# Kernel optimization log

Hardware: AMD Instinct MI355X
Metric: run time of the kernel (lower is better)

The kernel has to match this reference:

```python
import jax, jax.numpy as jnp
import numpy as np

H, HD = 4, 32      # num_heads, head_dim
EPS = 1e-6         # flax LayerNorm default epsilon


def _ln(x, s, b):
    mu = jnp.mean(x, -1, keepdims=True)
    var = jnp.var(x, -1, keepdims=True)
    return (x - mu) * jax.lax.rsqrt(var + EPS) * s + b


def _pos_enc(T, D, dtype):
    # standard sinusoidal time-series positional encoding
    pos = jnp.arange(T, dtype=jnp.float32)[:, None]
    div = jnp.exp(-jnp.log(10000.0) * jnp.arange(0, D, 2, dtype=jnp.float32) / D)
    ang = pos * div
    pe = jnp.zeros((T, D), jnp.float32).at[:, 0::2].set(jnp.sin(ang)).at[:, 1::2].set(jnp.cos(ang))
    return pe.astype(dtype)


def _transformer(x, Wi, bi, Wqkv, bqkv, Wo, bo, l1s, l1b, l2s, l2b, W1, b1, W2, b2):
    # x: [B, T, in_dim] -> [B, T, D]; pre-LN transformer block with pos-enc
    B, T, _ = x.shape
    x = x @ Wi + bi
    D = x.shape[-1]
    x = x + _pos_enc(T, D, x.dtype)
    h = _ln(x, l1s, l1b)
    qkv = (h @ Wqkv + bqkv).reshape(B, T, 3, H, HD)
    q, k, v = qkv[:, :, 0], qkv[:, :, 1], qkv[:, :, 2]
    s = jnp.einsum('bthd,bshd->bhts', q, k) * (1.0 / np.sqrt(HD))
    o = jnp.einsum('bhts,bshd->bthd', jax.nn.softmax(s, -1), v).reshape(B, T, H * HD)
    x = x + (o @ Wo + bo)
    h = _ln(x, l2s, l2b)
    return x + jax.nn.gelu(h @ W1 + b1) @ W2 + b2


def _grand(h, Win, bin_, Wqk, bqk, Wout, bout, t_grid):
    # GRAND-style attention diffusion across node axis: dz/dt = (A(z) - I) z,
    # explicit Euler on the given time grid. h: [B, T, N, D]
    B, T, N, D = h.shape
    z = h @ Win + bin_
    dts = t_grid[1:] - t_grid[:-1]
    scale = 1.0 / np.sqrt(HD)
    for i in range(int(dts.shape[0])):
        qk = (z @ Wqk + bqk).reshape(B, T, N, 2, H, HD)
        q, k = qk[:, :, :, 0], qk[:, :, :, 1]
        s = jnp.einsum('btnhd,btmhd->bthnm', q, k) * scale
        A = jax.nn.softmax(s, -1).mean(axis=2)  # head-averaged [B, T, N, N]
        z = z + dts[i] * (jnp.einsum('btnm,btmd->btnd', A, z) - z)
    return z @ Wout + bout


def _forward(x, tt_Wi, tt_bi, tt_Wqkv, tt_bqkv, tt_Wo, tt_bo, tt_ln1s, tt_ln1b,
             tt_ln2s, tt_ln2b, tt_W1, tt_b1, tt_W2, tt_b2,
             g_Win, g_bin, g_Wqk, g_bqk, g_Wout, g_bout,
             ln_s, ln_b, mW1, mb1, mW2, mb2):
    # per-channel temporal transformer: vmap over node axis 2, params axis 0
    tmodel = jax.vmap(_transformer, in_axes=(2,) + (0,) * 14, out_axes=2)
    h = tmodel(x, tt_Wi, tt_bi, tt_Wqkv, tt_bqkv, tt_Wo, tt_bo,
               tt_ln1s, tt_ln1b, tt_ln2s, tt_ln2b, tt_W1, tt_b1, tt_W2, tt_b2)
    t_grid = jnp.linspace(0.0, 0.5, 4)
    h = _grand(h, g_Win, g_bin, g_Wqk, g_bqk, g_Wout, g_bout, t_grid)
    h2 = _ln(h, ln_s, ln_b)
    return jax.nn.gelu(h2 @ mW1 + mb1) @ mW2 + mb2


def setup_inputs() -> dict:
    key = jax.random.key(0)
    ks = iter(jax.random.split(key, 32))
    B, T, N, IN, D = 8, 128, 64, 32, 128
    w = lambda shape: jax.random.normal(next(ks), shape, jnp.float32) * 0.02
    z = lambda shape: jnp.zeros(shape, jnp.float32)
    o = lambda shape: jnp.ones(shape, jnp.float32)
    return dict(
        x=jax.random.normal(next(ks), (B, T, N, IN), jnp.float32),
        tt_Wi=w((N, IN, D)), tt_bi=z((N, D)),
        tt_Wqkv=w((N, D, 3 * H * HD)), tt_bqkv=z((N, 3 * H * HD)),
        tt_Wo=w((N, H * HD, D)), tt_bo=z((N, D)),
        tt_ln1s=o((N, D)), tt_ln1b=z((N, D)),
        tt_ln2s=o((N, D)), tt_ln2b=z((N, D)),
        tt_W1=w((N, D, D)), tt_b1=z((N, D)),
        tt_W2=w((N, D, D)), tt_b2=z((N, D)),
        g_Win=w((D, D)), g_bin=z((D,)),
        g_Wqk=w((D, 2 * H * HD)), g_bqk=z((2 * H * HD,)),
        g_Wout=w((D, D)), g_bout=z((D,)),
        ln_s=o((D,)), ln_b=z((D,)),
        mW1=w((D, D)), mb1=z((D,)),
        mW2=w((D, D)), mb2=z((D,)),
    )


def reference(x, tt_Wi, tt_bi, tt_Wqkv, tt_bqkv, tt_Wo, tt_bo, tt_ln1s, tt_ln1b,
              tt_ln2s, tt_ln2b, tt_W1, tt_b1, tt_W2, tt_b2,
              g_Win, g_bin, g_Wqk, g_bqk, g_Wout, g_bout,
              ln_s, ln_b, mW1, mb1, mW2, mb2):
    return _forward(x, tt_Wi, tt_bi, tt_Wqkv, tt_bqkv, tt_Wo, tt_bo, tt_ln1s, tt_ln1b,
                    tt_ln2s, tt_ln2b, tt_W1, tt_b1, tt_W2, tt_b2,
                    g_Win, g_bin, g_Wqk, g_bqk, g_Wout, g_bout,
                    ln_s, ln_b, mW1, mb1, mW2, mb2)
```

## Files before the change

kernel.cpp:

```cpp
#include <hip/hip_runtime.h>
#include <hip/hip_bf16.h>

using bf16 = __hip_bfloat16;
typedef __attribute__((ext_vector_type(8))) short short8;
typedef __attribute__((ext_vector_type(4))) float f32x4;


__device__ __forceinline__ bool isbf(const void* p) {
    return *(const unsigned*)p == 0x3F803F80u;
}
template <bool BF>
__device__ __forceinline__ float ldT(const void* p, size_t i) {
    if constexpr (BF) return __bfloat162float(((const bf16*)p)[i]);
    else              return ((const float*)p)[i];
}
template <bool BF>
__device__ __forceinline__ void stT(void* p, size_t i, float v) {
    if constexpr (BF) ((bf16*)p)[i] = __float2bfloat16(v);
    else              ((float*)p)[i] = v;
}
template <bool BF>
__device__ __forceinline__ unsigned ldbits(const void* p, size_t i) {
    if constexpr (BF) return ((const unsigned short*)p)[i];
    else {
// ... 50 lines not shown
            sq  += e[kk][j] * e[kk][j];
        }
    }
    sum += __shfl_xor(sum, 16); sum += __shfl_xor(sum, 32);
    sq  += __shfl_xor(sq, 16);  sq  += __shfl_xor(sq, 32);
    float mu = sum * (1.0f / 128.0f);
    float var = sq * (1.0f / 128.0f) - mu * mu;
    float rs = rsqrtf(var + 1e-6f);
#pragma unroll
    for (int kk = 0; kk < 4; ++kk) {
        unsigned dw[4];
#pragma unroll
        for (int p = 0; p < 4; ++p) {
            int col = 32 * kk + 8 * lg + 2 * p;
            float2 sv = ld2T<BF>(lnsP, pb + col);
            float2 bv = ld2T<BF>(lnbP, pb + col);
            dw[p] = pack2((e[kk][2 * p]     - mu) * rs * sv.x + bv.x,
                          (e[kk][2 * p + 1] - mu) * rs * sv.y + bv.y);
        }
        af[kk] = u4_to_s8(make_uint4(dw[0], dw[1], dw[2], dw[3]));
    }
}

template <bool BF>
__device__ __forceinline__ void repack_body(const void* __restrict__ W,
                                            uint4* __restrict__ Wf, int Nout) {
    int kk = blockIdx.x, nt = blockIdx.y, node = blockIdx.z;
    int KK = gridDim.x, NT = gridDim.y;
    int l = threadIdx.x, lg = l >> 4, li = l & 15;
    int col = nt * 16 + li;
    int k0 = kk * 32 + lg * 8;
    size_t base = (size_t)node * (KK * 32) * Nout;
    unsigned w[4];
#pragma unroll
    for (int p = 0; p < 4; ++p) {
        unsigned lo = ldbits<BF>(W, base + (size_t)(k0 + 2 * p) * Nout + col);
        unsigned hi = ldbits<BF>(W, base + (size_t)(k0 + 2 * p + 1) * Nout + col);
        w[p] = lo | (hi << 16);
    }
    Wf[(((size_t)node * NT + nt) * KK + kk) * 64 + l] =
        make_uint4(w[0], w[1], w[2], w[3]);
}
__global__ __launch_bounds__(64) void k_repack(const void* W, uint4* Wf,
                                               int Nout, const void* probe) {
    if (isbf(probe)) repack_body<true>(W, Wf, Nout);
    else             repack_body<false>(W, Wf, Nout);
}

template <bool LNIN, bool GELU, bool ADD, int OM, bool PERMIN, bool PERM, bool BF>
__device__ __forceinline__ void mgemm_body(
    const uint4* __restrict__ A, const float* __restrict__ Af,
    const void* __restrict__ lnsP, const void* __restrict__ lnbP, int lnPerNode,
    const uint4* __restrict__ Wf, const void* __restrict__ Bias,
    const float* __restrict__ AddF, float* __restrict__ OutF,
    void* __restrict__ OutB, int Nout, int NT, int nodeW, int nodeB)
{
    int n64 = blockIdx.y, node = blockIdx.z;
    int row_base = blockIdx.z * 1024 + blockIdx.x * 64;
    int l = threadIdx.x, lg = l >> 4, li = l & 15;
    int wnode = nodeW ? node : 0;

    short8 bfrag[4][4];
    const uint4* wp = Wf + (((size_t)wnode * NT + n64 * 4) * 4) * 64 + l;
#pragma unroll
    for (int nt = 0; nt < 4; ++nt)
#pragma unroll
        for (int kk = 0; kk < 4; ++kk)
            bfrag[nt][kk] = u4_to_s8(wp[(nt * 4 + kk) * 64]);

    float bias[4];
#pragma unroll
    for (int nt = 0; nt < 4; ++nt)
        bias[nt] = ldT<BF>(Bias, (size_t)(nodeB ? node : 0) * Nout +
                                     n64 * 64 + nt * 16 + li);

#pragma unroll
    for (int m4 = 0; m4 < 4; ++m4) {
        int arow = row_base + m4 * 16 + li;
        short8 af[4];
        if constexpr (LNIN) {
            int xrow = PERMIN ? ((arow & 1023) * 64 + (arow >> 10)) : arow;
            ln_afrags<BF>(Af + (size_t)xrow * 128, lnsP, lnbP,
                          (size_t)(lnPerNode ? node : 0) * 128, lg, af);
        } else {
            const uint4* ap = A + (size_t)arow * 16;
#pragma unroll
            for (int kk = 0; kk < 4; ++kk) af[kk] = u4_to_s8(ap[kk * 4 + lg]);
        }
        f32x4 acc[4];
#pragma unroll
        for (int nt = 0; nt < 4; ++nt) {
            acc[nt] = (f32x4){0.f, 0.f, 0.f, 0.f};
#pragma unroll
            for (int kk = 0; kk < 4; ++kk)
                acc[nt] = __builtin_amdgcn_mfma_f32_16x16x32_bf16(
                    af[kk], bfrag[nt][kk], acc[nt], 0, 0, 0);
        }
#pragma unroll
        for (int nt = 0; nt < 4; ++nt) {
            int j = n64 * 64 + nt * 16 + li;
#pragma unroll
            for (int s = 0; s < 4; ++s) {
                int orow = row_base + m4 * 16 + (lg << 2) + s;
                int r_out = PERM ? ((orow & 1023) * 64 + (orow >> 10)) : orow;
                size_t oi = (size_t)r_out * Nout + j;
                float v = acc[nt][s] + bias[nt];
                if constexpr (ADD) v += AddF[oi];
                if constexpr (GELU) v = gelu_f(v);
                if constexpr (OM == 0) OutF[oi] = v;
                else if constexpr (OM == 1) ((bf16*)OutB)[oi] = f2b(v);
                else if constexpr (OM == 2) { OutF[oi] = v; ((bf16*)OutB)[oi] = f2b(v); }
                else stT<BF>(OutB, oi, v);
            }
        }
    }
}
template <bool LNIN, bool GELU, bool ADD, int OM, bool PERMIN, bool PERM>
__global__ __launch_bounds__(64) void k_mgemm(
    const uint4* A, const float* Af, const void* lnsP, const void* lnbP,
    int lnPerNode, const uint4* Wf, const void* Bias, const float* AddF,
    float* OutF, void* OutB, int Nout, int NT, int nodeW, int nodeB,
    const void* probe)
{
    if (isbf(probe))
        mgemm_body<LNIN, GELU, ADD, OM, PERMIN, PERM, true>(
            A, Af, lnsP, lnbP, lnPerNode, Wf, Bias, AddF, OutF, OutB, Nout, NT, nodeW, nodeB);
    else
        mgemm_body<LNIN, GELU, ADD, OM, PERMIN, PERM, false>(
            A, Af, lnsP, lnbP, lnPerNode, Wf, Bias, AddF, OutF, OutB, Nout, NT, nodeW, nodeB);
}

template <bool BF>
__device__ __forceinline__ void qkv_body(
    const float* __restrict__ X, const void* __restrict__ l1s,
    const void* __restrict__ l1b, const uint4* __restrict__ Wf,
    const void* __restrict__ Bias, unsigned short* __restrict__ Out)
{
    int tile = blockIdx.x, node = blockIdx.z;
    int l = threadIdx.x, lg = l >> 4, li = l & 15;

    short8 af[4][4];
#pragma unroll
    for (int m4 = 0; m4 < 4; ++m4) {
        int q = tile * 64 + m4 * 16 + li;
        ln_afrags<BF>(X + ((size_t)q * 64 + node) * 128, l1s, l1b,
                      (size_t)node * 128, lg, af[m4]);
    }
#pragma unroll
    for (int ct = 0; ct < 6; ++ct) {
        short8 bfr[4][4];
        float bias[4];
#pragma unroll
        for (int nt = 0; nt < 4; ++nt) {
#pragma unroll
            for (int kk = 0; kk < 4; ++kk)
                bfr[nt][kk] = u4_to_s8(Wf[(((size_t)node * 24 + ct * 4 + nt) * 4 + kk) * 64 + l]);
            bias[nt] = ldT<BF>(Bias, (size_t)node * 384 + ct * 64 + nt * 16 + li);
        }
#pragma unroll
        for (int m4 = 0; m4 < 4; ++m4) {
            f32x4 acc[4];
#pragma unroll
            for (int nt = 0; nt < 4; ++nt) {
                acc[nt] = (f32x4){0.f, 0.f, 0.f, 0.f};
#pragma unroll
                for (int kk = 0; kk < 4; ++kk)
                    acc[nt] = __builtin_amdgcn_mfma_f32_16x16x32_bf16(
                        af[m4][kk], bfr[nt][kk], acc[nt], 0, 0, 0);
            }
#pragma unroll
            for (int nt = 0; nt < 4; ++nt) {
                int j = ct * 64 + nt * 16 + li;
#pragma unroll
                for (int s = 0; s < 4; ++s) {
                    int orow = node * 1024 + tile * 64 + m4 * 16 + (lg << 2) + s;
                    Out[(size_t)orow * 384 + j] = f2bu(acc[nt][s] + bias[nt]);
                }
            }
        }
    }
}
__global__ __launch_bounds__(64) void k_qkv(
    const float* X, const void* l1s, const void* l1b, const uint4* Wf,
    const void* Bias, unsigned short* Out, const void* probe)
{
    if (isbf(probe)) qkv_body<true>(X, l1s, l1b, Wf, Bias, Out);
    else             qkv_body<false>(X, l1s, l1b, Wf, Bias, Out);
}

template <bool BF>
__device__ __forceinline__ void ffn_body(
    float* __restrict__ X, const void* __restrict__ l2s,
    const void* __restrict__ l2b, const uint4* __restrict__ W1f,
    const void* __restrict__ b1, const uint4* __restrict__ W2f,
    const void* __restrict__ b2, const uint4* __restrict__ Ginf,
    const void* __restrict__ gbin, unsigned short* __restrict__ Hs,
    unsigned short* __restrict__ Rs)
{
    int tile = blockIdx.x, node = blockIdx.z;
    int tid = threadIdx.x;
    int w = tid >> 6;
    int l = tid & 63, lg = l >> 4, li = l & 15;

    {
        short8 bfr[4][4];
        float bias[4];
#pragma unroll
        for (int nt = 0; nt < 4; ++nt) {
#pragma unroll
            for (int kk = 0; kk < 4; ++kk)
                bfr[nt][kk] = u4_to_s8(W1f[(((size_t)node * 8 + w * 4 + nt) * 4 + kk) * 64 + l]);
            bias[nt] = ldT<BF>(b1, (size_t)node * 128 + 64 * w + nt * 16 + li);
        }
#pragma unroll
        for (int m4 = 0; m4 < 4; ++m4) {
            int q = tile * 64 + m4 * 16 + li;
            short8 af[4];
            ln_afrags<BF>(X + ((size_t)q * 64 + node) * 128, l2s, l2b,
                          (size_t)node * 128, lg, af);
            f32x4 acc[4];
#pragma unroll
            for (int nt = 0; nt < 4; ++nt) {
                acc[nt] = (f32x4){0.f, 0.f, 0.f, 0.f};
#pragma unroll
                for (int kk = 0; kk < 4; ++kk)
                    acc[nt] = __builtin_amdgcn_mfma_f32_16x16x32_bf16(
                        af[kk], bfr[nt][kk], acc[nt], 0, 0, 0);
            }
#pragma unroll
            for (int nt = 0; nt < 4; ++nt) {
                int j = 64 * w + nt * 16 + li;
#pragma unroll
                for (int s = 0; s < 4; ++s) {
                    int row = m4 * 16 + (lg << 2) + s;
                    Hs[row * 128 + (j ^ ((row & 7) << 3))] =
                        f2bu(gelu_f(acc[nt][s] + bias[nt]));
                }
            }
        }
    }
    __syncthreads();
    {
        short8 bfr[4][4];
        float bias[4];
#pragma unroll
        for (int nt = 0; nt < 4; ++nt) {
#pragma unroll
            for (int kk = 0; kk < 4; ++kk)
                bfr[nt][kk] = u4_to_s8(W2f[(((size_t)node * 8 + w * 4 + nt) * 4 + kk) * 64 + l]);
            bias[nt] = ldT<BF>(b2, (size_t)node * 128 + 64 * w + nt * 16 + li);
        }
#pragma unroll
        for (int m4 = 0; m4 < 4; ++m4) {
            short8 af[4];
#pragma unroll
            for (int kk = 0; kk < 4; ++kk)
                af[kk] = u4_to_s8(*(const uint4*)&Hs[(16 * m4 + li) * 128 +
                                 ((32 * kk + 8 * lg) ^ ((li & 7) << 3))]);
            f32x4 acc[4];
#pragma unroll
            for (int nt = 0; nt < 4; ++nt) {
                acc[nt] = (f32x4){0.f, 0.f, 0.f, 0.f};
#pragma unroll
                for (int kk = 0; kk < 4; ++kk)
                    acc[nt] = __builtin_amdgcn_mfma_f32_16x16x32_bf16(
                        af[kk], bfr[nt][kk], acc[nt], 0, 0, 0);
            }
#pragma unroll
            for (int nt = 0; nt < 4; ++nt) {
                int j = 64 * w + nt * 16 + li;
#pragma unroll
                for (int s = 0; s < 4; ++s) {
                    int row = m4 * 16 + (lg << 2) + s;
                    int q = tile * 64 + row;
                    float v = acc[nt][s] + bias[nt] +
                              X[((size_t)q * 64 + node) * 128 + j];
                    Rs[row * 128 + (j ^ ((row & 7) << 3))] = f2bu(v);
                }
            }
        }
    }
    __syncthreads();
    {
        short8 bfr[4][4];
        float bias[4];
#pragma unroll
        for (int nt = 0; nt < 4; ++nt) {
#pragma unroll
            for (int kk = 0; kk < 4; ++kk)
                bfr[nt][kk] = u4_to_s8(Ginf[(((size_t)(w * 4 + nt)) * 4 + kk) * 64 + l]);
            bias[nt] = ldT<BF>(gbin, 64 * w + nt * 16 + li);
        }
#pragma unroll
        for (int m4 = 0; m4 < 4; ++m4) {
            short8 af[4];
#pragma unroll
            for (int kk = 0; kk < 4; ++kk)
                af[kk] = u4_to_s8(*(const uint4*)&Rs[(16 * m4 + li) * 128 +
                                 ((32 * kk + 8 * lg) ^ ((li & 7) << 3))]);
            f32x4 acc[4];
#pragma unroll
            for (int nt = 0; nt < 4; ++nt) {
                acc[nt] = (f32x4){0.f, 0.f, 0.f, 0.f};
#pragma unroll
                for (int kk = 0; kk < 4; ++kk)
                    acc[nt] = __builtin_amdgcn_mfma_f32_16x16x32_bf16(
                        af[kk], bfr[nt][kk], acc[nt], 0, 0, 0);
            }
#pragma unroll
            for (int nt = 0; nt < 4; ++nt) {
                int j = 64 * w + nt * 16 + li;
#pragma unroll
                for (int s = 0; s < 4; ++s) {
                    int row = m4 * 16 + (lg << 2) + s;
                    int q = tile * 64 + row;
                    X[((size_t)q * 64 + node) * 128 + j] = acc[nt][s] + bias[nt];
                }
            }
        }
    }
}
__global__ __launch_bounds__(128) void k_ffn(
    float* X, const void* l2s, const void* l2b, const uint4* W1f,
    const void* b1, const uint4* W2f, const void* b2, const uint4* Ginf,
    const void* gbin, const void* probe)
{
    __shared__ unsigned short Hs[64 * 128];
    __shared__ unsigned short Rs[64 * 128];
    if (isbf(probe)) ffn_body<true>(X, l2s, l2b, W1f, b1, W2f, b2, Ginf, gbin, Hs, Rs);
    else             ffn_body<false>(X, l2s, l2b, W1f, b1, W2f, b2, Ginf, gbin, Hs, Rs);
}

template <bool BF>
__device__ __forceinline__ void head_body(
    const float* __restrict__ X, const void* __restrict__ lns,
    const void* __restrict__ lnb, const uint4* __restrict__ M1f,
    const void* __restrict__ mb1, const uint4* __restrict__ M2f,
    const void* __restrict__ mb2, void* __restrict__ Out,
    unsigned short* __restrict__ Hs)
{
    int row_base = blockIdx.x * 64;
    int tid = threadIdx.x;
    int w = tid >> 6;
    int l = tid & 63, lg = l >> 4, li = l & 15;

    {
        short8 bfr[4][4];
        float bias[4];
#pragma unroll
        for (int nt = 0; nt < 4; ++nt) {
#pragma unroll
            for (int kk = 0; kk < 4; ++kk)
                bfr[nt][kk] = u4_to_s8(M1f[(((size_t)(w * 4 + nt)) * 4 + kk) * 64 + l]);
            bias[nt] = ldT<BF>(mb1, 64 * w + nt * 16 + li);
        }
#pragma unroll
        for (int m4 = 0; m4 < 4; ++m4) {
            int arow = row_base + m4 * 16 + li;
            short8 af[4];
            ln_afrags<BF>(X + (size_t)arow * 128, lns, lnb, 0, lg, af);
            f32x4 acc[4];
#pragma unroll
            for (int nt = 0; nt < 4; ++nt) {
                acc[nt] = (f32x4){0.f, 0.f, 0.f, 0.f};
#pragma unroll
                for (int kk = 0; kk < 4; ++kk)
                    acc[nt] = __builtin_amdgcn_mfma_f32_16x16x32_bf16(
                        af[kk], bfr[nt][kk], acc[nt], 0, 0, 0);
            }
#pragma unroll
            for (int nt = 0; nt < 4; ++nt) {
                int j = 64 * w + nt * 16 + li;
#pragma unroll
                for (int s = 0; s < 4; ++s) {
                    int row = m4 * 16 + (lg << 2) + s;
                    Hs[row * 128 + (j ^ ((row & 7) << 3))] =
                        f2bu(gelu_f(acc[nt][s] + bias[nt]));
                }
            }
        }
    }
    __syncthreads();
    {
        short8 bfr[4][4];
        float bias[4];
#pragma unroll
        for (int nt = 0; nt < 4; ++nt) {
#pragma unroll
            for (int kk = 0; kk < 4; ++kk)
                bfr[nt][kk] = u4_to_s8(M2f[(((size_t)(w * 4 + nt)) * 4 + kk) * 64 + l]);
            bias[nt] = ldT<BF>(mb2, 64 * w + nt * 16 + li);
        }
#pragma unroll
        for (int m4 = 0; m4 < 4; ++m4) {
            short8 af[4];
#pragma unroll
            for (int kk = 0; kk < 4; ++kk)
                af[kk] = u4_to_s8(*(const uint4*)&Hs[(16 * m4 + li) * 128 +
                                 ((32 * kk + 8 * lg) ^ ((li & 7) << 3))]);
            f32x4 acc[4];
#pragma unroll
            for (int nt = 0; nt < 4; ++nt) {
                acc[nt] = (f32x4){0.f, 0.f, 0.f, 0.f};
#pragma unroll
                for (int kk = 0; kk < 4; ++kk)
                    acc[nt] = __builtin_amdgcn_mfma_f32_16x16x32_bf16(
                        af[kk], bfr[nt][kk], acc[nt], 0, 0, 0);
            }
#pragma unroll
            for (int nt = 0; nt < 4; ++nt) {
                int j = 64 * w + nt * 16 + li;
#pragma unroll
                for (int s = 0; s < 4; ++s) {
                    int orow = row_base + m4 * 16 + (lg << 2) + s;
                    stT<BF>(Out, (size_t)orow * 128 + j, acc[nt][s] + bias[nt]);
                }
            }
        }
    }
}
__global__ __launch_bounds__(128) void k_head(
    const float* X, const void* lns, const void* lnb, const uint4* M1f,
    const void* mb1, const uint4* M2f, const void* mb2, void* Out,
    const void* probe)
{
    __shared__ unsigned short Hs[64 * 128];
    if (isbf(probe)) head_body<true>(X, lns, lnb, M1f, mb1, M2f, mb2, Out, Hs);
    else             head_body<false>(X, lns, lnb, M1f, mb1, M2f, mb2, Out, Hs);
}

__global__ __launch_bounds__(128) void k_pe(float* __restrict__ pe) {
    int t = blockIdx.x, d = threadIdx.x;
    float div = expf(-9.210340371976184f * (float)(d & ~1) * (1.0f / 128.0f));
    float ang = (float)t * div;
    pe[t * 128 + d] = (d & 1) ? cosf(ang) : sinf(ang);
}

template <bool BF>
__device__ __forceinline__ void inproj_mfma_body(
    const void* __restrict__ x, const uint4* __restrict__ WfWi,
    const void* __restrict__ bi, const float* __restrict__ pe,
    float* __restrict__ X)
{
    int tile = blockIdx.x, n64 = blockIdx.y, node = blockIdx.z;
    int l = threadIdx.x, lg = l >> 4, li = l & 15;

    short8 bfrag[4];
    float bias[4];
#pragma unroll
    for (int nt = 0; nt < 4; ++nt) {
        bfrag[nt] = u4_to_s8(WfWi[((size_t)node * 8 + n64 * 4 + nt) * 64 + l]);
        bias[nt] = ldT<BF>(bi, (size_t)node * 128 + n64 * 64 + nt * 16 + li);
    }

#pragma unroll
    for (int mt = 0; mt < 4; ++mt) {
        int q = tile * 64 + mt * 16 + li;
        size_t xoff = ((size_t)q * 64 + node) * 32 + 8 * lg;
// ... 120 lines not shown
                int src = (2 * (lg & 1) + (j >> 1)) * 16 + li;
                unsigned v0 = (unsigned)__shfl((int)pdw[2 * kc][j & 1], src);
                unsigned v1 = (unsigned)__shfl((int)pdw[2 * kc + 1][j & 1], src);
                bd[j] = (lg & 2) ? v1 : v0;
            }
            short8 pf = u4_to_s8(make_uint4(bd[0], bd[1], bd[2], bd[3]));
            o0 = __builtin_amdgcn_mfma_f32_16x16x32_bf16(vf[0][kc], pf, o0, 0, 0, 0);
            o1 = __builtin_amdgcn_mfma_f32_16x16x32_bf16(vf[1][kc], pf, o1, 0, 0, 0);
        }
        float linv = 1.0f / lsum;
        size_t obase = ((size_t)n * 1024 + b * 128 + st * 16 + li) * 128 + h * 32;
        uint2 w0, w1;
        w0.x = pack2(o0[0] * linv, o0[1] * linv);
        w0.y = pack2(o0[2] * linv, o0[3] * linv);
        w1.x = pack2(o1[0] * linv, o1[1] * linv);
        w1.y = pack2(o1[2] * linv, o1[3] * linv);
        *(uint2*)((unsigned short*)O + obase + 4 * lg)      = w0;
        *(uint2*)((unsigned short*)O + obase + 16 + 4 * lg) = w1;
    }
}

template <bool BF>
__device__ __forceinline__ void grand_fused_body(
    const float* __restrict__ Xf, const uint4* __restrict__ Wqk,
    const void* __restrict__ bqk, bf16* __restrict__ Zout,
    unsigned short* __restrict__ Zb, unsigned short* __restrict__ QKs)
{
    int bt = blockIdx.x;
    int tid = threadIdx.x;
    int w = tid >> 6;
    int h = w >> 1, wh = w & 1;
    int l = tid & 63, lg = l >> 4, li = l & 15;
    const float scale = 0.17677669529663687f;
    const float dtv = 0.16666667f;
    const int dcol = 16 * w + li;

    float zreg[4][4];
#pragma unroll
    for (int nt = 0; nt < 4; ++nt)
#pragma unroll
        for (int s = 0; s < 4; ++s) {
            int n = 16 * nt + 4 * lg + s;
            float z = Xf[((size_t)bt * 64 + n) * 128 + dcol];
            zreg[nt][s] = z;
            Zb[n * 128 + (dcol ^ ((n & 7) << 3))] = f2bu(z);
        }
    float bias[2];
#pragma unroll
// ... 119 lines not shown
#pragma unroll
        for (int hh = 0; hh < 4; ++hh)
#pragma unroll
            for (int kk = 0; kk < 2; ++kk)
#pragma unroll
                for (int nt = 0; nt < 4; ++nt) {
                    short8 af = u4_to_s8(*(const uint4*)&QKs[(16 * nt + li) * 256 +
                                 ((64 * hh + 32 * kk + 8 * lg) ^ ((li & 7) << 3))]);
                    oz[nt] = __builtin_amdgcn_mfma_f32_16x16x32_bf16(
                        af, bz[kk], oz[nt], 0, 0, 0);
                }
#pragma unroll
        for (int nt = 0; nt < 4; ++nt)
#pragma unroll
            for (int s = 0; s < 4; ++s) {
                int n = 16 * nt + 4 * lg + s;
                float z = zreg[nt][s];
                float zn = z + dtv * (oz[nt][s] - z);
                zreg[nt][s] = zn;
                Zb[n * 128 + (dcol ^ ((n & 7) << 3))] = f2bu(zn);
            }
        __syncthreads();
    }
    for (int idx = tid; idx < 1024; idx += 512) {
        int row = idx >> 4, c = idx & 15;
        uint4 v = *(const uint4*)&Zb[row * 128 + ((c * 8) ^ ((row & 7) << 3))];
        ((uint4*)Zout)[((size_t)bt * 64 + row) * 16 + c] = v;
    }
}
__global__ __launch_bounds__(512, 2) void k_grand_fused(
    const float* Xf, const uint4* Wqk, const void* bqk, bf16* Zout,
    const void* probe)
{
    __shared__ unsigned short Zb[64 * 128];
    __shared__ unsigned short QKs[64 * 256];
    if (isbf(probe)) grand_fused_body<true>(Xf, Wqk, bqk, Zout, Zb, QKs);
    else             grand_fused_body<false>(Xf, Wqk, bqk, Zout, Zb, QKs);
}

extern "C" void kernel_launch(void* const* d_in, const int* in_sizes, int n_in,
                              void* d_out, int out_size, void* d_ws, size_t ws_size,
                              hipStream_t stream)
{
    const void* x     = d_in[0];
    const void* tWi   = d_in[1];
    const void* tbi   = d_in[2];
    const void* tWqkv = d_in[3];
    const void* tbqkv = d_in[4];
    const void* tWo   = d_in[5];
    const void* tbo   = d_in[6];
    const void* l1s   = d_in[7];
    const void* l1b   = d_in[8];
    const void* l2s   = d_in[9];
    const void* l2b   = d_in[10];
    const void* tW1   = d_in[11];
    const void* tb1   = d_in[12];
    const void* tW2   = d_in[13];
    const void* tb2   = d_in[14];
    const void* gWin  = d_in[15];
    const void* gbin  = d_in[16];
    const void* gWqk  = d_in[17];
    const void* gbqk  = d_in[18];
    const void* gWout = d_in[19];
    const void* gbout = d_in[20];
    const void* lns   = d_in[21];
    const void* lnb   = d_in[22];
    const void* mW1   = d_in[23];
    const void* mb1   = d_in[24];
    const void* mW2   = d_in[25];
    const void* mb2   = d_in[26];
    const void* probe = lns;

    const size_t MiB = 1u << 20;
    char* ws = (char*)d_ws;

    float* X   = (float*)ws;
    float* pe  = (float*)(ws + 61 * MiB);
    bf16*  S16 = (bf16*)(ws + 64 * MiB);
    bf16*  bfB = (bf16*)(ws + 96 * MiB);
    bf16*  bfA = (bf16*)(ws + 112 * MiB);

    char* wf = ws + 32 * MiB;
    uint4* WfQKV = (uint4*)(wf);
    uint4* WfWo  = (uint4*)(wf + 6291456);
    uint4* WfW1  = (uint4*)(wf + 8388608);
    uint4* WfW2  = (uint4*)(wf + 10485760);
    uint4* WfGin = (uint4*)(wf + 12582912);
    uint4* WfGqk = (uint4*)(wf + 12615680);
    uint4* WfGout= (uint4*)(wf + 12681216);
    uint4* WfM1  = (uint4*)(wf + 12713984);
    uint4* WfM2  = (uint4*)(wf + 12746752);
    uint4* WfWi  = (uint4*)(wf + 12779520);

    k_repack<<<dim3(4, 24, 64), 64, 0, stream>>>(tWqkv, WfQKV, 384, probe);
    k_repack<<<dim3(4, 8, 64), 64, 0, stream>>>(tWo,  WfWo,  128, probe);
    k_repack<<<dim3(4, 8, 64), 64, 0, stream>>>(tW1,  WfW1,  128, probe);
    k_repack<<<dim3(4, 8, 64), 64, 0, stream>>>(tW2,  WfW2,  128, probe);
    k_repack<<<dim3(4, 8, 1),  64, 0, stream>>>(gWin, WfGin, 128, probe);
    k_repack<<<dim3(4, 16, 1), 64, 0, stream>>>(gWqk, WfGqk, 256, probe);
    k_repack<<<dim3(4, 8, 1),  64, 0, stream>>>(gWout,WfGout,128, probe);
    k_repack<<<dim3(4, 8, 1),  64, 0, stream>>>(mW1,  WfM1,  128, probe);
    k_repack<<<dim3(4, 8, 1),  64, 0, stream>>>(mW2,  WfM2,  128, probe);
    k_repack<<<dim3(1, 8, 64), 64, 0, stream>>>(tWi,  WfWi,  128, probe);
    k_pe<<<128, 128, 0, stream>>>(pe);

    k_inproj_mfma<<<dim3(16, 2, 64), 64, 0, stream>>>(x, WfWi, tbi, pe, X, probe);
    k_qkv<<<dim3(16, 1, 64), 64, 0, stream>>>(
        X, l1s, l1b, WfQKV, tbqkv, (unsigned short*)S16, probe);
    k_attn<<<2048, 128, 0, stream>>>((const unsigned short*)S16, bfA);
    k_mgemm<false, false, true, 0, false, true><<<dim3(16, 2, 64), 64, 0, stream>>>(
        (const uint4*)bfA, nullptr, nullptr, nullptr, 0,
        WfWo, tbo, X, X, nullptr, 128, 8, 1, 1, probe);
    k_ffn<<<dim3(16, 1, 64), 128, 0, stream>>>(
        X, l2s, l2b, WfW1, tb1, WfW2, tb2, WfGin, gbin, probe);

    k_grand_fused<<<1024, 512, 0, stream>>>(X, WfGqk, gbqk, bfB, probe);
    k_mgemm<false, false, false, 0, false, false><<<dim3(1024, 2, 1), 64, 0, stream>>>(
        (const uint4*)bfB, nullptr, nullptr, nullptr, 0,
        WfGout, gbout, nullptr, X, nullptr, 128, 8, 0, 0, probe);

    k_head<<<1024, 128, 0, stream>>>(
        X, lns, lnb, WfM1, mb1, WfM2, mb2, d_out, probe);
}
```

Baseline: 250.9 us.

## Merge prep kernels, fuse Gout GEMM into GRAND, widen FFN/head/QKV grids

Replaces the ten weight-repack launches and the positional-encoding launch with a single prep kernel that dispatches on block index. The GRAND output projection now runs inside the fused GRAND kernel straight from the shared-memory Z tile, which removes the bf16 round trip through global memory and one launch. The FFN and head kernels move from 128 to 256 threads, each wave covering two 16-column tiles, and QKV uses 16-row tiles on a four-times larger grid. This raises parallelism at the cost of reloading weight fragments more often per row.

```diff
diff --git a/kernel.cpp b/kernel.cpp
--- a/kernel.cpp
+++ b/kernel.cpp
@@ -96,15 +96,42 @@
     }
 }
 
-template <bool BF>
-__device__ __forceinline__ void repack_body(const void* __restrict__ W,
-                                            uint4* __restrict__ Wf, int Nout) {
-    int kk = blockIdx.x, nt = blockIdx.y, node = blockIdx.z;
-    int KK = gridDim.x, NT = gridDim.y;
-    int l = threadIdx.x, lg = l >> 4, li = l & 15;
+struct PrepArgs {
+    const void* W[10];
+    uint4* Wf[10];
+    float* pe;
+};
+__device__ __constant__ const int prep_KK[10]    = {4,4,4,4,4,4,4,4,4,1};
+__device__ __constant__ const int prep_NT[10]    = {24,8,8,8,8,16,8,8,8,8};
+__device__ __constant__ const int prep_start[11] =
+    {0,6144,8192,10240,12288,12320,12384,12416,12448,12480,12992};
+
+template <bool BF>
+__device__ __forceinline__ void prep_body(PrepArgs a) {
+    int bid = blockIdx.x;
+    int l = threadIdx.x;
+    if (bid >= 12992) {
+        int t = bid - 12992;
+        int d = l * 2;
+        float div0 = expf(-9.210340371976184f * (float)(d & ~1) * (1.0f / 128.0f));
+        float ang = (float)t * div0;
+        *(float2*)(a.pe + t * 128 + d) = make_float2(sinf(ang), cosf(ang));
+        return;
+    }
+    int seg = 0;
+#pragma unroll
+    for (int s = 1; s < 10; ++s) seg += (bid >= prep_start[s]);
+    int local = bid - prep_start[seg];
+    int KK = prep_KK[seg], NT = prep_NT[seg];
+    int kk = local % KK;
+    int nt = (local / KK) % NT;
+    int node = local / (KK * NT);
+    int Nout = NT * 16;
+    int lg = l >> 4, li = l & 15;
     int col = nt * 16 + li;
     int k0 = kk * 32 + lg * 8;
     size_t base = (size_t)node * (KK * 32) * Nout;
+    const void* W = a.W[seg];
     unsigned w[4];
 #pragma unroll
     for (int p = 0; p < 4; ++p) {
@@ -112,22 +139,19 @@
         unsigned hi = ldbits<BF>(W, base + (size_t)(k0 + 2 * p + 1) * Nout + col);
         w[p] = lo | (hi << 16);
     }
-    Wf[(((size_t)node * NT + nt) * KK + kk) * 64 + l] =
+    a.Wf[seg][(((size_t)node * NT + nt) * KK + kk) * 64 + l] =
         make_uint4(w[0], w[1], w[2], w[3]);
 }
-__global__ __launch_bounds__(64) void k_repack(const void* W, uint4* Wf,
-                                               int Nout, const void* probe) {
-    if (isbf(probe)) repack_body<true>(W, Wf, Nout);
-    else             repack_body<false>(W, Wf, Nout);
-}
-
-template <bool LNIN, bool GELU, bool ADD, int OM, bool PERMIN, bool PERM, bool BF>
+__global__ __launch_bounds__(64) void k_prep(PrepArgs a, const void* probe) {
+    if (isbf(probe)) prep_body<true>(a);
+    else             prep_body<false>(a);
+}
+
+template <bool ADD, bool PERM, bool BF>
 __device__ __forceinline__ void mgemm_body(
-    const uint4* __restrict__ A, const float* __restrict__ Af,
-    const void* __restrict__ lnsP, const void* __restrict__ lnbP, int lnPerNode,
-    const uint4* __restrict__ Wf, const void* __restrict__ Bias,
-    const float* __restrict__ AddF, float* __restrict__ OutF,
-    void* __restrict__ OutB, int Nout, int NT, int nodeW, int nodeB)
+    const uint4* __restrict__ A, const uint4* __restrict__ Wf,
+    const void* __restrict__ Bias, const float* __restrict__ AddF,
+    float* __restrict__ OutF, int Nout, int NT, int nodeW, int nodeB)
 {
     int n64 = blockIdx.y, node = blockIdx.z;
     int row_base = blockIdx.z * 1024 + blockIdx.x * 64;
@@ -152,15 +176,9 @@
     for (int m4 = 0; m4 < 4; ++m4) {
         int arow = row_base + m4 * 16 + li;
         short8 af[4];
-        if constexpr (LNIN) {
-            int xrow = PERMIN ? ((arow & 1023) * 64 + (arow >> 10)) : arow;
-            ln_afrags<BF>(Af + (size_t)xrow * 128, lnsP, lnbP,
-                          (size_t)(lnPerNode ? node : 0) * 128, lg, af);
-        } else {
-            const uint4* ap = A + (size_t)arow * 16;
-#pragma unroll
-            for (int kk = 0; kk < 4; ++kk) af[kk] = u4_to_s8(ap[kk * 4 + lg]);
-        }
+        const uint4* ap = A + (size_t)arow * 16;
+#pragma unroll
+        for (int kk = 0; kk < 4; ++kk) af[kk] = u4_to_s8(ap[kk * 4 + lg]);
         f32x4 acc[4];
 #pragma unroll
         for (int nt = 0; nt < 4; ++nt) {
@@ -180,28 +198,20 @@
                 size_t oi = (size_t)r_out * Nout + j;
                 float v = acc[nt][s] + bias[nt];
                 if constexpr (ADD) v += AddF[oi];
-                if constexpr (GELU) v = gelu_f(v);
-                if constexpr (OM == 0) OutF[oi] = v;
-                else if constexpr (OM == 1) ((bf16*)OutB)[oi] = f2b(v);
-                else if constexpr (OM == 2) { OutF[oi] = v; ((bf16*)OutB)[oi] = f2b(v); }
-                else stT<BF>(OutB, oi, v);
-            }
-        }
-    }
-}
-template <bool LNIN, bool GELU, bool ADD, int OM, bool PERMIN, bool PERM>
+                OutF[oi] = v;
+            }
+        }
+    }
+}
+template <bool ADD, bool PERM>
 __global__ __launch_bounds__(64) void k_mgemm(
-    const uint4* A, const float* Af, const void* lnsP, const void* lnbP,
-    int lnPerNode, const uint4* Wf, const void* Bias, const float* AddF,
-    float* OutF, void* OutB, int Nout, int NT, int nodeW, int nodeB,
-    const void* probe)
+    const uint4* A, const uint4* Wf, const void* Bias, const float* AddF,
+    float* OutF, int Nout, int NT, int nodeW, int nodeB, const void* probe)
 {
     if (isbf(probe))
-        mgemm_body<LNIN, GELU, ADD, OM, PERMIN, PERM, true>(
-            A, Af, lnsP, lnbP, lnPerNode, Wf, Bias, AddF, OutF, OutB, Nout, NT, nodeW, nodeB);
+        mgemm_body<ADD, PERM, true>(A, Wf, Bias, AddF, OutF, Nout, NT, nodeW, nodeB);
     else
-        mgemm_body<LNIN, GELU, ADD, OM, PERMIN, PERM, false>(
-            A, Af, lnsP, lnbP, lnPerNode, Wf, Bias, AddF, OutF, OutB, Nout, NT, nodeW, nodeB);
+        mgemm_body<ADD, PERM, false>(A, Wf, Bias, AddF, OutF, Nout, NT, nodeW, nodeB);
 }
 
 template <bool BF>
@@ -210,46 +220,32 @@
     const void* __restrict__ l1b, const uint4* __restrict__ Wf,
     const void* __restrict__ Bias, unsigned short* __restrict__ Out)
 {
-    int tile = blockIdx.x, node = blockIdx.z;
+    int tile16 = blockIdx.x, node = blockIdx.z;
     int l = threadIdx.x, lg = l >> 4, li = l & 15;
-
-    short8 af[4][4];
-#pragma unroll
-    for (int m4 = 0; m4 < 4; ++m4) {
-        int q = tile * 64 + m4 * 16 + li;
-        ln_afrags<BF>(X + ((size_t)q * 64 + node) * 128, l1s, l1b,
-                      (size_t)node * 128, lg, af[m4]);
-    }
+    int q = tile16 * 16 + li;
+
+    short8 af[4];
+    ln_afrags<BF>(X + ((size_t)q * 64 + node) * 128, l1s, l1b,
+                  (size_t)node * 128, lg, af);
 #pragma unroll
     for (int ct = 0; ct < 6; ++ct) {
-        short8 bfr[4][4];
-        float bias[4];
 #pragma unroll
         for (int nt = 0; nt < 4; ++nt) {
-#pragma unroll
-            for (int kk = 0; kk < 4; ++kk)
-                bfr[nt][kk] = u4_to_s8(Wf[(((size_t)node * 24 + ct * 4 + nt) * 4 + kk) * 64 + l]);
-            bias[nt] = ldT<BF>(Bias, (size_t)node * 384 + ct * 64 + nt * 16 + li);
-        }
-#pragma unroll
-        for (int m4 = 0; m4 < 4; ++m4) {
-            f32x4 acc[4];
-#pragma unroll
-            for (int nt = 0; nt < 4; ++nt) {
-                acc[nt] = (f32x4){0.f, 0.f, 0.f, 0.f};
-#pragma unroll
-                for (int kk = 0; kk < 4; ++kk)
-                    acc[nt] = __builtin_amdgcn_mfma_f32_16x16x32_bf16(
-                        af[m4][kk], bfr[nt][kk], acc[nt], 0, 0, 0);
-            }
-#pragma unroll
-            for (int nt = 0; nt < 4; ++nt) {
-                int j = ct * 64 + nt * 16 + li;
-#pragma unroll
-                for (int s = 0; s < 4; ++s) {
-                    int orow = node * 1024 + tile * 64 + m4 * 16 + (lg << 2) + s;
-                    Out[(size_t)orow * 384 + j] = f2bu(acc[nt][s] + bias[nt]);
-                }
+            short8 bfr[4];
+#pragma unroll
+            for (int kk = 0; kk < 4; ++kk)
+                bfr[kk] = u4_to_s8(Wf[(((size_t)node * 24 + ct * 4 + nt) * 4 + kk) * 64 + l]);
+            float bias = ldT<BF>(Bias, (size_t)node * 384 + ct * 64 + nt * 16 + li);
+            f32x4 acc = (f32x4){0.f, 0.f, 0.f, 0.f};
+#pragma unroll
+            for (int kk = 0; kk < 4; ++kk)
+                acc = __builtin_amdgcn_mfma_f32_16x16x32_bf16(
+                    af[kk], bfr[kk], acc, 0, 0, 0);
+            int j = ct * 64 + nt * 16 + li;
+#pragma unroll
+            for (int s = 0; s < 4; ++s) {
+                int orow = node * 1024 + tile16 * 16 + (lg << 2) + s;
+                Out[(size_t)orow * 384 + j] = f2bu(acc[s] + bias);
             }
         }
     }
@@ -276,125 +272,97 @@
     int w = tid >> 6;
     int l = tid & 63, lg = l >> 4, li = l & 15;
 
-    {
-        short8 bfr[4][4];
-        float bias[4];
-#pragma unroll
-        for (int nt = 0; nt < 4; ++nt) {
-#pragma unroll
-            for (int kk = 0; kk < 4; ++kk)
-                bfr[nt][kk] = u4_to_s8(W1f[(((size_t)node * 8 + w * 4 + nt) * 4 + kk) * 64 + l]);
-            bias[nt] = ldT<BF>(b1, (size_t)node * 128 + 64 * w + nt * 16 + li);
-        }
-#pragma unroll
-        for (int m4 = 0; m4 < 4; ++m4) {
-            int q = tile * 64 + m4 * 16 + li;
-            short8 af[4];
-            ln_afrags<BF>(X + ((size_t)q * 64 + node) * 128, l2s, l2b,
-                          (size_t)node * 128, lg, af);
-            f32x4 acc[4];
-#pragma unroll
-            for (int nt = 0; nt < 4; ++nt) {
-                acc[nt] = (f32x4){0.f, 0.f, 0.f, 0.f};
-#pragma unroll
-                for (int kk = 0; kk < 4; ++kk)
-                    acc[nt] = __builtin_amdgcn_mfma_f32_16x16x32_bf16(
-                        af[kk], bfr[nt][kk], acc[nt], 0, 0, 0);
-            }
-#pragma unroll
-            for (int nt = 0; nt < 4; ++nt) {
-                int j = 64 * w + nt * 16 + li;
-#pragma unroll
-                for (int s = 0; s < 4; ++s) {
-                    int row = m4 * 16 + (lg << 2) + s;
-                    Hs[row * 128 + (j ^ ((row & 7) << 3))] =
-                        f2bu(gelu_f(acc[nt][s] + bias[nt]));
-                }
+#pragma unroll
+    for (int m4 = 0; m4 < 4; ++m4) {
+        int q = tile * 64 + m4 * 16 + li;
+        short8 af[4];
+        ln_afrags<BF>(X + ((size_t)q * 64 + node) * 128, l2s, l2b,
+                      (size_t)node * 128, lg, af);
+#pragma unroll
+        for (int t2 = 0; t2 < 2; ++t2) {
+            int nt = 2 * w + t2;
+            short8 bfr[4];
+#pragma unroll
+            for (int kk = 0; kk < 4; ++kk)
+                bfr[kk] = u4_to_s8(W1f[(((size_t)node * 8 + nt) * 4 + kk) * 64 + l]);
+            float bias = ldT<BF>(b1, (size_t)node * 128 + nt * 16 + li);
+            f32x4 acc = (f32x4){0.f, 0.f, 0.f, 0.f};
+#pragma unroll
+            for (int kk = 0; kk < 4; ++kk)
+                acc = __builtin_amdgcn_mfma_f32_16x16x32_bf16(
+                    af[kk], bfr[kk], acc, 0, 0, 0);
+            int j = nt * 16 + li;
+#pragma unroll
+            for (int s = 0; s < 4; ++s) {
+                int row = m4 * 16 + (lg << 2) + s;
+                Hs[row * 128 + (j ^ ((row & 7) << 3))] =
+                    f2bu(gelu_f(acc[s] + bias));
             }
         }
     }
     __syncthreads();
-    {
-        short8 bfr[4][4];
-        float bias[4];
-#pragma unroll
-        for (int nt = 0; nt < 4; ++nt) {
-#pragma unroll
-            for (int kk = 0; kk < 4; ++kk)
-                bfr[nt][kk] = u4_to_s8(W2f[(((size_t)node * 8 + w * 4 + nt) * 4 + kk) * 64 + l]);
-            bias[nt] = ldT<BF>(b2, (size_t)node * 128 + 64 * w + nt * 16 + li);
-        }
-#pragma unroll
-        for (int m4 = 0; m4 < 4; ++m4) {
-            short8 af[4];
-#pragma unroll
-            for (int kk = 0; kk < 4; ++kk)
-                af[kk] = u4_to_s8(*(const uint4*)&Hs[(16 * m4 + li) * 128 +
-                                 ((32 * kk + 8 * lg) ^ ((li & 7) << 3))]);
-            f32x4 acc[4];
-#pragma unroll
-            for (int nt = 0; nt < 4; ++nt) {
-                acc[nt] = (f32x4){0.f, 0.f, 0.f, 0.f};
-#pragma unroll
-                for (int kk = 0; kk < 4; ++kk)
-                    acc[nt] = __builtin_amdgcn_mfma_f32_16x16x32_bf16(
-                        af[kk], bfr[nt][kk], acc[nt], 0, 0, 0);
-            }
-#pragma unroll
-            for (int nt = 0; nt < 4; ++nt) {
-                int j = 64 * w + nt * 16 + li;
-#pragma unroll
-                for (int s = 0; s < 4; ++s) {
-                    int row = m4 * 16 + (lg << 2) + s;
-                    int q = tile * 64 + row;
-                    float v = acc[nt][s] + bias[nt] +
-                              X[((size_t)q * 64 + node) * 128 + j];
-                    Rs[row * 128 + (j ^ ((row & 7) << 3))] = f2bu(v);
-                }
+#pragma unroll
+    for (int m4 = 0; m4 < 4; ++m4) {
+        short8 af[4];
+#pragma unroll
+        for (int kk = 0; kk < 4; ++kk)
+            af[kk] = u4_to_s8(*(const uint4*)&Hs[(16 * m4 + li) * 128 +
+                             ((32 * kk + 8 * lg) ^ ((li & 7) << 3))]);
+#pragma unroll
+        for (int t2 = 0; t2 < 2; ++t2) {
+            int nt = 2 * w + t2;
+            short8 bfr[4];
+#pragma unroll
+            for (int kk = 0; kk < 4; ++kk)
+                bfr[kk] = u4_to_s8(W2f[(((size_t)node * 8 + nt) * 4 + kk) * 64 + l]);
+            float bias = ldT<BF>(b2, (size_t)node * 128 + nt * 16 + li);
+            f32x4 acc = (f32x4){0.f, 0.f, 0.f, 0.f};
+#pragma unroll
+            for (int kk = 0; kk < 4; ++kk)
+                acc = __builtin_amdgcn_mfma_f32_16x16x32_bf16(
+                    af[kk], bfr[kk], acc, 0, 0, 0);
+            int j = nt * 16 + li;
+#pragma unroll
+            for (int s = 0; s < 4; ++s) {
+                int row = m4 * 16 + (lg << 2) + s;
+                int q = tile * 64 + row;
+                float v = acc[s] + bias + X[((size_t)q * 64 + node) * 128 + j];
+                Rs[row * 128 + (j ^ ((row & 7) << 3))] = f2bu(v);
             }
         }
     }
     __syncthreads();
-    {
-        short8 bfr[4][4];
-        float bias[4];
-#pragma unroll
-        for (int nt = 0; nt < 4; ++nt) {
-#pragma unroll
-            for (int kk = 0; kk < 4; ++kk)
-                bfr[nt][kk] = u4_to_s8(Ginf[(((size_t)(w * 4 + nt)) * 4 + kk) * 64 + l]);
-            bias[nt] = ldT<BF>(gbin, 64 * w + nt * 16 + li);
-        }
-#pragma unroll
-        for (int m4 = 0; m4 < 4; ++m4) {
-            short8 af[4];
-#pragma unroll
-            for (int kk = 0; kk < 4; ++kk)
-                af[kk] = u4_to_s8(*(const uint4*)&Rs[(16 * m4 + li) * 128 +
-                                 ((32 * kk + 8 * lg) ^ ((li & 7) << 3))]);
-            f32x4 acc[4];
-#pragma unroll
-            for (int nt = 0; nt < 4; ++nt) {
-                acc[nt] = (f32x4){0.f, 0.f, 0.f, 0.f};
-#pragma unroll
-                for (int kk = 0; kk < 4; ++kk)
-                    acc[nt] = __builtin_amdgcn_mfma_f32_16x16x32_bf16(
-                        af[kk], bfr[nt][kk], acc[nt], 0, 0, 0);
-            }
-#pragma unroll
-            for (int nt = 0; nt < 4; ++nt) {
-                int j = 64 * w + nt * 16 + li;
-#pragma unroll
-                for (int s = 0; s < 4; ++s) {
-                    int row = m4 * 16 + (lg << 2) + s;
-                    int q = tile * 64 + row;
-                    X[((size_t)q * 64 + node) * 128 + j] = acc[nt][s] + bias[nt];
-                }
-            }
-        }
-    }
-}
-__global__ __launch_bounds__(128) void k_ffn(
+#pragma unroll
+    for (int m4 = 0; m4 < 4; ++m4) {
+        short8 af[4];
+#pragma unroll
+        for (int kk = 0; kk < 4; ++kk)
+            af[kk] = u4_to_s8(*(const uint4*)&Rs[(16 * m4 + li) * 128 +
+                             ((32 * kk + 8 * lg) ^ ((li & 7) << 3))]);
+#pragma unroll
+        for (int t2 = 0; t2 < 2; ++t2) {
+            int nt = 2 * w + t2;
+            short8 bfr[4];
+#pragma unroll
+            for (int kk = 0; kk < 4; ++kk)
+                bfr[kk] = u4_to_s8(Ginf[((size_t)nt * 4 + kk) * 64 + l]);
+            float bias = ldT<BF>(gbin, nt * 16 + li);
+            f32x4 acc = (f32x4){0.f, 0.f, 0.f, 0.f};
+#pragma unroll
+            for (int kk = 0; kk < 4; ++kk)
+                acc = __builtin_amdgcn_mfma_f32_16x16x32_bf16(
+                    af[kk], bfr[kk], acc, 0, 0, 0);
+            int j = nt * 16 + li;
+#pragma unroll
+            for (int s = 0; s < 4; ++s) {
+                int row = m4 * 16 + (lg << 2) + s;
+                int q = tile * 64 + row;
+                X[((size_t)q * 64 + node) * 128 + j] = acc[s] + bias;
+            }
+        }
+    }
+}
+__global__ __launch_bounds__(256) void k_ffn(
     float* X, const void* l2s, const void* l2b, const uint4* W1f,
     const void* b1, const uint4* W2f, const void* b2, const uint4* Ginf,
     const void* gbin, const void* probe)
@@ -418,82 +386,64 @@
     int w = tid >> 6;
     int l = tid & 63, lg = l >> 4, li = l & 15;
 
-    {
-        short8 bfr[4][4];
-        float bias[4];
-#pragma unroll
-        for (int nt = 0; nt < 4; ++nt) {
-#pragma unroll
-            for (int kk = 0; kk < 4; ++kk)
-                bfr[nt][kk] = u4_to_s8(M1f[(((size_t)(w * 4 + nt)) * 4 + kk) * 64 + l]);
-            bias[nt] = ldT<BF>(mb1, 64 * w + nt * 16 + li);
-        }
-#pragma unroll
-        for (int m4 = 0; m4 < 4; ++m4) {
-            int arow = row_base + m4 * 16 + li;
-            short8 af[4];
-            ln_afrags<BF>(X + (size_t)arow * 128, lns, lnb, 0, lg, af);
-            f32x4 acc[4];
-#pragma unroll
-            for (int nt = 0; nt < 4; ++nt) {
-                acc[nt] = (f32x4){0.f, 0.f, 0.f, 0.f};
-#pragma unroll
-                for (int kk = 0; kk < 4; ++kk)
-                    acc[nt] = __builtin_amdgcn_mfma_f32_16x16x32_bf16(
-                        af[kk], bfr[nt][kk], acc[nt], 0, 0, 0);
-            }
-#pragma unroll
-            for (int nt = 0; nt < 4; ++nt) {
-                int j = 64 * w + nt * 16 + li;
-#pragma unroll
-                for (int s = 0; s < 4; ++s) {
-                    int row = m4 * 16 + (lg << 2) + s;
-                    Hs[row * 128 + (j ^ ((row & 7) << 3))] =
-                        f2bu(gelu_f(acc[nt][s] + bias[nt]));
-                }
+#pragma unroll
+    for (int m4 = 0; m4 < 4; ++m4) {
+        int arow = row_base + m4 * 16 + li;
+        short8 af[4];
+        ln_afrags<BF>(X + (size_t)arow * 128, lns, lnb, 0, lg, af);
+#pragma unroll
+        for (int t2 = 0; t2 < 2; ++t2) {
+            int nt = 2 * w + t2;
+            short8 bfr[4];
+#pragma unroll
+            for (int kk = 0; kk < 4; ++kk)
+                bfr[kk] = u4_to_s8(M1f[((size_t)nt * 4 + kk) * 64 + l]);
+            float bias = ldT<BF>(mb1, nt * 16 + li);
+            f32x4 acc = (f32x4){0.f, 0.f, 0.f, 0.f};
+#pragma unroll
+            for (int kk = 0; kk < 4; ++kk)
+                acc = __builtin_amdgcn_mfma_f32_16x16x32_bf16(
+                    af[kk], bfr[kk], acc, 0, 0, 0);
+            int j = nt * 16 + li;
+#pragma unroll
+            for (int s = 0; s < 4; ++s) {
+                int row = m4 * 16 + (lg << 2) + s;
+                Hs[row * 128 + (j ^ ((row & 7) << 3))] =
+                    f2bu(gelu_f(acc[s] + bias));
             }
         }
     }
     __syncthreads();
-    {
-        short8 bfr[4][4];
-        float bias[4];
-#pragma unroll
-        for (int nt = 0; nt < 4; ++nt) {
-#pragma unroll
-            for (int kk = 0; kk < 4; ++kk)
-                bfr[nt][kk] = u4_to_s8(M2f[(((size_t)(w * 4 + nt)) * 4 + kk) * 64 + l]);
-            bias[nt] = ldT<BF>(mb2, 64 * w + nt * 16 + li);
-        }
-#pragma unroll
-        for (int m4 = 0; m4 < 4; ++m4) {
-            short8 af[4];
-#pragma unroll
-            for (int kk = 0; kk < 4; ++kk)
-                af[kk] = u4_to_s8(*(const uint4*)&Hs[(16 * m4 + li) * 128 +
-                                 ((32 * kk + 8 * lg) ^ ((li & 7) << 3))]);
-            f32x4 acc[4];
-#pragma unroll
-            for (int nt = 0; nt < 4; ++nt) {
-                acc[nt] = (f32x4){0.f, 0.f, 0.f, 0.f};
-#pragma unroll
-                for (int kk = 0; kk < 4; ++kk)
-                    acc[nt] = __builtin_amdgcn_mfma_f32_16x16x32_bf16(
-                        af[kk], bfr[nt][kk], acc[nt], 0, 0, 0);
-            }
-#pragma unroll
-            for (int nt = 0; nt < 4; ++nt) {
-                int j = 64 * w + nt * 16 + li;
-#pragma unroll
-                for (int s = 0; s < 4; ++s) {
-                    int orow = row_base + m4 * 16 + (lg << 2) + s;
-                    stT<BF>(Out, (size_t)orow * 128 + j, acc[nt][s] + bias[nt]);
-                }
-            }
-        }
-    }
-}
-__global__ __launch_bounds__(128) void k_head(
+#pragma unroll
+    for (int m4 = 0; m4 < 4; ++m4) {
+        short8 af[4];
+#pragma unroll
+        for (int kk = 0; kk < 4; ++kk)
+            af[kk] = u4_to_s8(*(const uint4*)&Hs[(16 * m4 + li) * 128 +
+                             ((32 * kk + 8 * lg) ^ ((li & 7) << 3))]);
+#pragma unroll
+        for (int t2 = 0; t2 < 2; ++t2) {
+            int nt = 2 * w + t2;
+            short8 bfr[4];
+#pragma unroll
+            for (int kk = 0; kk < 4; ++kk)
+                bfr[kk] = u4_to_s8(M2f[((size_t)nt * 4 + kk) * 64 + l]);
+            float bias = ldT<BF>(mb2, nt * 16 + li);
+            f32x4 acc = (f32x4){0.f, 0.f, 0.f, 0.f};
+#pragma unroll
+            for (int kk = 0; kk < 4; ++kk)
+                acc = __builtin_amdgcn_mfma_f32_16x16x32_bf16(
+                    af[kk], bfr[kk], acc, 0, 0, 0);
+            int j = nt * 16 + li;
+#pragma unroll
+            for (int s = 0; s < 4; ++s) {
+                int orow = row_base + m4 * 16 + (lg << 2) + s;
+                stT<BF>(Out, (size_t)orow * 128 + j, acc[s] + bias);
+            }
+        }
+    }
+}
+__global__ __launch_bounds__(256) void k_head(
     const float* X, const void* lns, const void* lnb, const uint4* M1f,
     const void* mb1, const uint4* M2f, const void* mb2, void* Out,
     const void* probe)
@@ -501,13 +451,6 @@
     __shared__ unsigned short Hs[64 * 128];
     if (isbf(probe)) head_body<true>(X, lns, lnb, M1f, mb1, M2f, mb2, Out, Hs);
     else             head_body<false>(X, lns, lnb, M1f, mb1, M2f, mb2, Out, Hs);
-}
-
-__global__ __launch_bounds__(128) void k_pe(float* __restrict__ pe) {
-    int t = blockIdx.x, d = threadIdx.x;
-    float div = expf(-9.210340371976184f * (float)(d & ~1) * (1.0f / 128.0f));
-    float ang = (float)t * div;
-    pe[t * 128 + d] = (d & 1) ? cosf(ang) : sinf(ang);
 }
 
 template <bool BF>
@@ -674,8 +617,9 @@
 
 template <bool BF>
 __device__ __forceinline__ void grand_fused_body(
-    const float* __restrict__ Xf, const uint4* __restrict__ Wqk,
-    const void* __restrict__ bqk, bf16* __restrict__ Zout,
+    float* __restrict__ Xf, const uint4* __restrict__ Wqk,
+    const void* __restrict__ bqk, const uint4* __restrict__ Goutf,
+    const void* __restrict__ gbout,
     unsigned short* __restrict__ Zb, unsigned short* __restrict__ QKs)
 {
     int bt = blockIdx.x;
@@ -841,20 +785,40 @@
             }
         __syncthreads();
     }
-    for (int idx = tid; idx < 1024; idx += 512) {
-        int row = idx >> 4, c = idx & 15;
-        uint4 v = *(const uint4*)&Zb[row * 128 + ((c * 8) ^ ((row & 7) << 3))];
-        ((uint4*)Zout)[((size_t)bt * 64 + row) * 16 + c] = v;
+    {
+        short8 gb[4];
+#pragma unroll
+        for (int kk = 0; kk < 4; ++kk)
+            gb[kk] = u4_to_s8(Goutf[((size_t)w * 4 + kk) * 64 + l]);
+        float gbias = ldT<BF>(gbout, 16 * w + li);
+#pragma unroll
+        for (int mt = 0; mt < 4; ++mt) {
+            short8 af[4];
+#pragma unroll
+            for (int kk = 0; kk < 4; ++kk)
+                af[kk] = u4_to_s8(*(const uint4*)&Zb[(16 * mt + li) * 128 +
+                                 ((32 * kk + 8 * lg) ^ ((li & 7) << 3))]);
+            f32x4 acc = (f32x4){0.f, 0.f, 0.f, 0.f};
+#pragma unroll
+            for (int kk = 0; kk < 4; ++kk)
+                acc = __builtin_amdgcn_mfma_f32_16x16x32_bf16(
+                    af[kk], gb[kk], acc, 0, 0, 0);
+#pragma unroll
+            for (int s = 0; s < 4; ++s) {
+                int n = 16 * mt + 4 * lg + s;
+                Xf[((size_t)bt * 64 + n) * 128 + 16 * w + li] = acc[s] + gbias;
+            }
+        }
     }
 }
 __global__ __launch_bounds__(512, 2) void k_grand_fused(
-    const float* Xf, const uint4* Wqk, const void* bqk, bf16* Zout,
-    const void* probe)
+    float* Xf, const uint4* Wqk, const void* bqk, const uint4* Goutf,
+    const void* gbout, const void* probe)
 {
     __shared__ unsigned short Zb[64 * 128];
     __shared__ unsigned short QKs[64 * 256];
-    if (isbf(probe)) grand_fused_body<true>(Xf, Wqk, bqk, Zout, Zb, QKs);
-    else             grand_fused_body<false>(Xf, Wqk, bqk, Zout, Zb, QKs);
+    if (isbf(probe)) grand_fused_body<true>(Xf, Wqk, bqk, Goutf, gbout, Zb, QKs);
+    else             grand_fused_body<false>(Xf, Wqk, bqk, Goutf, gbout, Zb, QKs);
 }
 
 extern "C" void kernel_launch(void* const* d_in, const int* in_sizes, int n_in,
@@ -896,7 +860,6 @@
     float* X   = (float*)ws;
     float* pe  = (float*)(ws + 61 * MiB);
     bf16*  S16 = (bf16*)(ws + 64 * MiB);
-    bf16*  bfB = (bf16*)(ws + 96 * MiB);
     bf16*  bfA = (bf16*)(ws + 112 * MiB);
 
     char* wf = ws + 32 * MiB;
@@ -911,33 +874,31 @@
     uint4* WfM2  = (uint4*)(wf + 12746752);
     uint4* WfWi  = (uint4*)(wf + 12779520);
 
-    k_repack<<<dim3(4, 24, 64), 64, 0, stream>>>(tWqkv, WfQKV, 384, probe);
-    k_repack<<<dim3(4, 8, 64), 64, 0, stream>>>(tWo,  WfWo,  128, probe);
-    k_repack<<<dim3(4, 8, 64), 64, 0, stream>>>(tW1,  WfW1,  128, probe);
-    k_repack<<<dim3(4, 8, 64), 64, 0, stream>>>(tW2,  WfW2,  128, probe);
-    k_repack<<<dim3(4, 8, 1),  64, 0, stream>>>(gWin, WfGin, 128, probe);
-    k_repack<<<dim3(4, 16, 1), 64, 0, stream>>>(gWqk, WfGqk, 256, probe);
-    k_repack<<<dim3(4, 8, 1),  64, 0, stream>>>(gWout,WfGout,128, probe);
-    k_repack<<<dim3(4, 8, 1),  64, 0, stream>>>(mW1,  WfM1,  128, probe);
-    k_repack<<<dim3(4, 8, 1),  64, 0, stream>>>(mW2,  WfM2,  128, probe);
-    k_repack<<<dim3(1, 8, 64), 64, 0, stream>>>(tWi,  WfWi,  128, probe);
-    k_pe<<<128, 128, 0, stream>>>(pe);
+    PrepArgs pa;
+    pa.W[0] = tWqkv; pa.Wf[0] = WfQKV;
+    pa.W[1] = tWo;   pa.Wf[1] = WfWo;
+    pa.W[2] = tW1;   pa.Wf[2] = WfW1;
+    pa.W[3] = tW2;   pa.Wf[3] = WfW2;
+    pa.W[4] = gWin;  pa.Wf[4] = WfGin;
+    pa.W[5] = gWqk;  pa.Wf[5] = WfGqk;
+    pa.W[6] = gWout; pa.Wf[6] = WfGout;
+    pa.W[7] = mW1;   pa.Wf[7] = WfM1;
+    pa.W[8] = mW2;   pa.Wf[8] = WfM2;
+    pa.W[9] = tWi;   pa.Wf[9] = WfWi;
+    pa.pe = pe;
+    k_prep<<<13120, 64, 0, stream>>>(pa, probe);
 
     k_inproj_mfma<<<dim3(16, 2, 64), 64, 0, stream>>>(x, WfWi, tbi, pe, X, probe);
-    k_qkv<<<dim3(16, 1, 64), 64, 0, stream>>>(
+    k_qkv<<<dim3(64, 1, 64), 64, 0, stream>>>(
         X, l1s, l1b, WfQKV, tbqkv, (unsigned short*)S16, probe);
     k_attn<<<2048, 128, 0, stream>>>((const unsigned short*)S16, bfA);
-    k_mgemm<false, false, true, 0, false, true><<<dim3(16, 2, 64), 64, 0, stream>>>(
-        (const uint4*)bfA, nullptr, nullptr, nullptr, 0,
-        WfWo, tbo, X, X, nullptr, 128, 8, 1, 1, probe);
-    k_ffn<<<dim3(16, 1, 64), 128, 0, stream>>>(
+    k_mgemm<true, true><<<dim3(16, 2, 64), 64, 0, stream>>>(
+        (const uint4*)bfA, WfWo, tbo, X, X, 128, 8, 1, 1, probe);
+    k_ffn<<<dim3(16, 1, 64), 256, 0, stream>>>(
         X, l2s, l2b, WfW1, tb1, WfW2, tb2, WfGin, gbin, probe);
 
-    k_grand_fused<<<1024, 512, 0, stream>>>(X, WfGqk, gbqk, bfB, probe);
-    k_mgemm<false, false, false, 0, false, false><<<dim3(1024, 2, 1), 64, 0, stream>>>(
-        (const uint4*)bfB, nullptr, nullptr, nullptr, 0,
-        WfGout, gbout, nullptr, X, nullptr, 128, 8, 0, 0, probe);
-
-    k_head<<<1024, 128, 0, stream>>>(
+    k_grand_fused<<<1024, 512, 0, stream>>>(X, WfGqk, gbqk, WfGout, gbout, probe);
+
+    k_head<<<1024, 256, 0, stream>>>(
         X, lns, lnb, WfM1, mb1, WfM2, mb2, d_out, probe);
 }
```

After: 259.9 us. 1.04x slower.
